# Optimization experiments

Measured on AMD Instinct MI355X. Metric: run time of the kernel, lower is better.

The kernel has to match this reference:

```python
import jax, jax.numpy as jnp
import numpy as np

DIM = 576
HEADS = 8
AGENT = 49
GRID_SIZE = 5
ORDER = 3
BN_EPS = 1e-5


def _kan_grid():
    h = 2.0 / GRID_SIZE  # grid_range [-1, 1]
    return jnp.arange(-ORDER, GRID_SIZE + ORDER + 1, dtype=jnp.float32) * h - 1.0


def _bsplines(x, grid):
    # x: (M, in) -> (M, in, GRID_SIZE + ORDER) Cox-de Boor B-spline bases (efficient-kan)
    xe = x[..., None]
    b = ((xe >= grid[:-1]) & (xe < grid[1:])).astype(x.dtype)
    for k in range(1, ORDER + 1):
        b = ((xe - grid[:-(k + 1)]) / (grid[k:-1] - grid[:-(k + 1)]) * b[..., :-1]
             + (grid[k + 1:] - xe) / (grid[k + 1:] - grid[1:-k]) * b[..., 1:])
    return b


def setup_inputs() -> dict:
    key = jax.random.key(0)
    ks = jax.random.split(key, 16)
    b, H, W = 32, 28, 28
    n, c = H * W, DIM
    nrm = lambda k, shape, std=0.02: jax.random.normal(k, shape, jnp.float32) * std
    return {
        "x": jax.random.normal(ks[0], (b, n, c), jnp.float32),
        "H": H,
        "W": W,
        "Wq": nrm(ks[1], (c, c)),
        "Wkv": nrm(ks[2], (2 * c, c)),
        "an_bias": nrm(ks[3], (HEADS, AGENT, 7, 7)),
        "na_bias": nrm(ks[4], (HEADS, AGENT, 7, 7)),
        "ah_bias": nrm(ks[5], (1, HEADS, AGENT, H, 1)),
        "aw_bias": nrm(ks[6], (1, HEADS, AGENT, 1, W)),
        "ha_bias": nrm(ks[7], (1, HEADS, H, 1, AGENT)),
        "wa_bias": nrm(ks[8], (1, HEADS, 1, W, AGENT)),
        "dwc_w": nrm(ks[9], (c, 1, 3, 3), 0.1),
        "dwc_b": jnp.zeros((c,), jnp.float32),
        "bn_gamma": jnp.ones((c,), jnp.float32),
        "bn_beta": jnp.zeros((c,), jnp.float32),
        "bn_mean": jnp.zeros((c,), jnp.float32),
        "bn_var": jnp.ones((c,), jnp.float32),
        "base_weight": nrm(ks[10], (c, c)),
        "spline_weight": nrm(ks[11], (c, c, GRID_SIZE + ORDER)),
        "spline_scaler": jnp.ones((c, c), jnp.float32),
    }


def reference(x, H, W, Wq, Wkv, an_bias, na_bias, ah_bias, aw_bias, ha_bias, wa_bias,
              dwc_w, dwc_b, bn_gamma, bn_beta, bn_mean, bn_var,
              base_weight, spline_weight, spline_scaler):
    b, n, c = x.shape
    h, hd = HEADS, c // HEADS
    scale = hd ** -0.5
    q = x @ Wq.T                       # (b,n,c)
    kv = x @ Wkv.T                     # (b,n,2c)  (sr_ratio == 1)
    k, v = kv[..., :c], kv[..., c:]
    # agent tokens: AdaptiveAvgPool2d(28x28 -> 7x7) == exact 4x4 mean pooling
    p = int(AGENT ** 0.5)
    agent = q.reshape(b, p, H // p, p, W // p, c).mean(axis=(2, 4)).reshape(b, AGENT, c)
    qh = q.reshape(b, n, h, hd).transpose(0, 2, 1, 3)       # (b,h,n,hd)
    kh = k.reshape(b, n, h, hd).transpose(0, 2, 1, 3)
    vh = v.reshape(b, n, h, hd).transpose(0, 2, 1, 3)
    ah = agent.reshape(b, AGENT, h, hd).transpose(0, 2, 1, 3)  # (b,h,A,hd)
    # stage 1: agent tokens attend to k/v (bilinear-upsampled 7x7 bias + separable bias)
    pb1 = jax.image.resize(an_bias, (h, AGENT, H, W), "bilinear").reshape(1, h, AGENT, n)
    pb2 = (ah_bias + aw_bias).reshape(1, h, AGENT, n)
    agent_attn = jax.nn.softmax(jnp.einsum("bhad,bhnd->bhan", ah * scale, kh) + pb1 + pb2, axis=-1)
    agent_v = jnp.einsum("bhan,bhnd->bhad", agent_attn, vh)    # (b,h,A,hd)
    # stage 2: queries attend to agent tokens
    ab1 = jax.image.resize(na_bias, (h, AGENT, H, W), "bilinear").reshape(1, h, AGENT, n).transpose(0, 1, 3, 2)
    ab2 = (ha_bias + wa_bias).reshape(1, h, n, AGENT)
    q_attn = jax.nn.softmax(jnp.einsum("bhnd,bhad->bhna", qh * scale, ah) + ab1 + ab2, axis=-1)
    out = jnp.einsum("bhna,bhad->bhnd", q_attn, agent_v).transpose(0, 2, 1, 3).reshape(b, n, c)
    # depthwise-conv + BN(eval) + ReLU residual on v
    vimg = v.transpose(0, 2, 1).reshape(b, c, H, W)
    y = jax.lax.conv_general_dilated(vimg, dwc_w, (1, 1), "SAME",
                                     feature_group_count=c,
                                     dimension_numbers=("NCHW", "OIHW", "NCHW"))
    y = y + dwc_b[None, :, None, None]
    scale_bn = (bn_gamma / jnp.sqrt(bn_var + BN_EPS))[None, :, None, None]
    y = (y - bn_mean[None, :, None, None]) * scale_bn + bn_beta[None, :, None, None]
    y = jax.nn.relu(y).reshape(b, c, n).transpose(0, 2, 1)
    out = out + y
    # KANLinear projection: silu base branch + B-spline branch
    xf = out.reshape(b * n, c)
    bases = _bsplines(xf, _kan_grid())                           # (M, in, 8)
    scaled = spline_weight * spline_scaler[..., None]            # (out, in, 8)
    proj = jax.nn.silu(xf) @ base_weight.T + jnp.einsum("mik,oik->mo", bases, scaled)
    return proj.reshape(b, n, c)
```

## Files before the change

kernel.cpp:

```cpp
#include <hip/hip_runtime.h>
#include <hip/hip_bf16.h>
#include <math.h>

#define B_ 32
#define N_ 784
#define C_ 576
#define H_ 28
#define W_ 28
#define HEADS_ 8
#define HD_ 72
#define AGENT_ 49
#define M_ (B_ * N_)
#define KTOT_ 5184
#define QKVW_ 1728
#define SCALE_ 0.11785113019775793f
#define LDA_ 40

typedef unsigned short ushort_t;
typedef __attribute__((ext_vector_type(8))) unsigned short u16x8;
typedef __attribute__((ext_vector_type(8))) __bf16 bf16x8;
typedef __attribute__((ext_vector_type(4))) float f32x4;
typedef __attribute__((ext_vector_type(4))) unsigned u32x4;

__device__ __forceinline__ ushort_t f2bf(float f) {
  union { float f; unsigned u; } v; v.f = f;
  unsigned r = v.u + 0x7fffu + ((v.u >> 16) & 1u);
  return (ushort_t)(r >> 16);
}
__device__ __forceinline__ float bf2f(ushort_t u) {
  union { unsigned u; float f; } v; v.u = ((unsigned)u) << 16;
  return v.f;
}
__device__ __forceinline__ unsigned pack2(float lo, float hi) {
  __bf16 a = (__bf16)lo, b = (__bf16)hi;
  unsigned short ua = __builtin_bit_cast(unsigned short, a);
  unsigned short ub = __builtin_bit_cast(unsigned short, b);
  return (unsigned)ua | ((unsigned)ub << 16);
}

__global__ __launch_bounds__(256) void convert_x_kernel(
    const float* __restrict__ x, ushort_t* __restrict__ xbf) {
  const int total8 = M_ * C_ / 8;
  for (int i = blockIdx.x * 256 + threadIdx.x; i < total8; i += gridDim.x * 256) {
    f32x4 a = *(const f32x4*)(x + i * 8);
    f32x4 b = *(const f32x4*)(x + i * 8 + 4);
    u16x8 o;
    o[0]=f2bf(a[0]); o[1]=f2bf(a[1]); o[2]=f2bf(a[2]); o[3]=f2bf(a[3]);
    o[4]=f2bf(b[0]); o[5]=f2bf(b[1]); o[6]=f2bf(b[2]); o[7]=f2bf(b[3]);
    *(u16x8*)(xbf + i * 8) = o;
  }
}

__global__ __launch_bounds__(256) void pack_w_kernel(
    const float* __restrict__ Wq, const float* __restrict__ Wkv,
    ushort_t* __restrict__ wbf) {
  int total = QKVW_ * C_;
  for (int i = blockIdx.x * 256 + threadIdx.x; i < total; i += gridDim.x * 256) {
    int j = i / C_, k = i % C_;
    float v = (j < C_) ? Wq[(size_t)j * C_ + k] : Wkv[(size_t)(j - C_) * C_ + k];
    wbf[i] = f2bf(v);
  }
}

__global__ __launch_bounds__(256) void pack_b_kernel(
    const float* __restrict__ base_w, const float* __restrict__ spline_w,
    const float* __restrict__ spline_s, ushort_t* __restrict__ bpackb) {
  int o = blockIdx.x;
  for (int j = threadIdx.x; j < KTOT_; j += 256) {
    float v;
    if (j < C_) {
      v = base_w[(size_t)o * C_ + j];
    } else {
      int jj = j - C_;
      int i = jj >> 3, kk = jj & 7;
      v = spline_w[((size_t)o * C_ + i) * 8 + kk] * spline_s[(size_t)o * C_ + i];
    }
    bpackb[(size_t)o * KTOT_ + j] = f2bf(v);
  }
}

__device__ __forceinline__ float bilerp7(const float* __restrict__ Bsrc, int y, int x) {
  float sy = y * 0.25f - 0.375f;
  float sx = x * 0.25f - 0.375f;
  float fy0 = floorf(sy), fx0 = floorf(sx);
  int y0 = (int)fy0, x0 = (int)fx0;
  float fy = sy - fy0, fx = sx - fx0;
  int y0c = min(6, max(0, y0)), y1c = min(6, max(0, y0 + 1));
  int x0c = min(6, max(0, x0)), x1c = min(6, max(0, x0 + 1));
  float v00 = Bsrc[y0c * 7 + x0c], v01 = Bsrc[y0c * 7 + x1c];
  float v10 = Bsrc[y1c * 7 + x0c], v11 = Bsrc[y1c * 7 + x1c];
  return (1.f - fy) * ((1.f - fx) * v00 + fx * v01)
       + fy * ((1.f - fx) * v10 + fx * v11);
}

__global__ __launch_bounds__(256) void bias_kernel(
    const float* __restrict__ an_bias, const float* __restrict__ na_bias,
    const float* __restrict__ ah_bias, const float* __restrict__ aw_bias,
    const float* __restrict__ ha_bias, const float* __restrict__ wa_bias,
    float* __restrict__ abias, float* __restrict__ qbias) {
  int idx = blockIdx.x * 256 + threadIdx.x;
  if (idx >= HEADS_ * AGENT_ * N_) return;
  int n = idx % N_;
  int ha = idx / N_;
  int h = ha / AGENT_, a = ha % AGENT_;
  int y = n / W_, x = n % W_;
  float pb1 = bilerp7(an_bias + (size_t)ha * 49, y, x);
  float pb2 = ah_bias[ha * H_ + y] + aw_bias[ha * W_ + x];
  abias[(size_t)ha * N_ + n] = pb1 + pb2;
  float ab1 = bilerp7(na_bias + (size_t)ha * 49, y, x);
  float ab2 = ha_bias[(h * H_ + y) * AGENT_ + a] + wa_bias[(h * W_ + x) * AGENT_ + a];
  qbias[((size_t)h * N_ + n) * AGENT_ + a] = ab1 + ab2;
}

__global__ __launch_bounds__(512, 4) void mfma_qkv_kernel(
    const ushort_t* __restrict__ A, const ushort_t* __restrict__ Bt,
    ushort_t* __restrict__ out) {
  __shared__ ushort_t Asl[2][128 * LDA_];
  __shared__ ushort_t Bsl[2][192 * LDA_];
  const int tid = threadIdx.x;
  const int lane = tid & 63, wid = tid >> 6;
  const int wm = wid >> 2, wn = wid & 3;
  const int l16 = lane & 15, lq = lane >> 4;

  int lin = blockIdx.x;
  const int q = 220, r = 4;
  int xcd = lin & 7;
  int wg = (xcd < r ? xcd * (q + 1) : r * (q + 1) + (xcd - r) * q) + (lin >> 3);
  const int m0 = (wg / 9) * 128, n0 = (wg % 9) * 192;

  const int rA = tid >> 2, hA = tid & 3;
  const int rB0 = tid >> 2, cB0 = tid & 3;
  const int rB1 = 128 + (tid >> 2), cB1 = tid & 3;
  const bool hasB1 = tid < 256;

  const ushort_t* arow = A + (size_t)(m0 + rA) * C_ + hA * 8;
  const ushort_t* brow0 = Bt + (size_t)(n0 + rB0) * C_ + cB0 * 8;
  const ushort_t* brow1 = Bt + (size_t)(n0 + rB1) * C_ + cB1 * 8;

  f32x4 acc[4][3] = {};
  u16x8 ar, br0, br1;

  ar = *(const u16x8*)(arow);
  br0 = *(const u16x8*)(brow0);
  if (hasB1) br1 = *(const u16x8*)(brow1);
  *(u16x8*)&Asl[0][rA * LDA_ + hA * 8] = ar;
  *(u16x8*)&Bsl[0][rB0 * LDA_ + cB0 * 8] = br0;
  if (hasB1) *(u16x8*)&Bsl[0][rB1 * LDA_ + cB1 * 8] = br1;
  ar = *(const u16x8*)(arow + 32);
  br0 = *(const u16x8*)(brow0 + 32);
  if (hasB1) br1 = *(const u16x8*)(brow1 + 32);
  __syncthreads();

  const int NSTEP = C_ / 32;
  for (int s = 0; s < NSTEP; ++s) {
    const int cur = s & 1;
    bf16x8 af[4], bfr[3];
    #pragma unroll
    for (int fm = 0; fm < 4; ++fm)
      af[fm] = *(const bf16x8*)&Asl[cur][(wm * 64 + fm * 16 + l16) * LDA_ + lq * 8];
    #pragma unroll
    for (int fn = 0; fn < 3; ++fn)
      bfr[fn] = *(const bf16x8*)&Bsl[cur][(wn * 48 + fn * 16 + l16) * LDA_ + lq * 8];
    #pragma unroll
    for (int fm = 0; fm < 4; ++fm)
      #pragma unroll
      for (int fn = 0; fn < 3; ++fn)
        acc[fm][fn] = __builtin_amdgcn_mfma_f32_16x16x32_bf16(
            af[fm], bfr[fn], acc[fm][fn], 0, 0, 0);
    if (s + 1 < NSTEP) {
      const int nxt = cur ^ 1;
      *(u16x8*)&Asl[nxt][rA * LDA_ + hA * 8] = ar;
      *(u16x8*)&Bsl[nxt][rB0 * LDA_ + cB0 * 8] = br0;
      if (hasB1) *(u16x8*)&Bsl[nxt][rB1 * LDA_ + cB1 * 8] = br1;
      if (s + 2 < NSTEP) {
        const int kl = (s + 2) * 32;
        ar = *(const u16x8*)(arow + kl);
        br0 = *(const u16x8*)(brow0 + kl);
        if (hasB1) br1 = *(const u16x8*)(brow1 + kl);
      }
    }
    __syncthreads();
  }
  #pragma unroll
  for (int fm = 0; fm < 4; ++fm) {
    #pragma unroll
    for (int fn = 0; fn < 3; ++fn) {
      int col = n0 + wn * 48 + fn * 16 + l16;
      #pragma unroll
      for (int r2 = 0; r2 < 4; ++r2) {
        int row = m0 + wm * 64 + fm * 16 + lq * 4 + r2;
        out[(size_t)row * QKVW_ + col] = f2bf(acc[fm][fn][r2]);
      }
    }
  }
}

__device__ __forceinline__ u32x4 basesPack(float xv) {
  float s = __fmaf_rn(xv, 2.5f, 5.5f);
  float tf = floorf(s);
  int t = (int)tf;
  float u = s - tf;
  float u2 = u * u, u3 = u2 * u, um = 1.f - u;
  float p0 = u3 * (1.f / 6.f);
  float p1 = (-3.f * u3 + 3.f * u2 + 3.f * u + 1.f) * (1.f / 6.f);
  float p2 = (3.f * u3 - 6.f * u2 + 4.f) * (1.f / 6.f);
  float p3 = um * um * um * (1.f / 6.f);
  unsigned lo = pack2(p3, p2);
  unsigned hi = pack2(p1, p0);
  unsigned cm1 = lo << 16;
  unsigned c1  = (lo >> 16) | (hi << 16);
  unsigned c3  = hi >> 16;
  bool inr = (t >= 0) && (t <= 10);
  u32x4 o;
  #pragma unroll
  for (int j = 0; j < 4; ++j) {
    int d = 3 - t + 2 * j;
    unsigned rr = 0u;
    rr = (d == -1) ? cm1 : rr;
    rr = (d == 0)  ? lo  : rr;
    rr = (d == 1)  ? c1  : rr;
    rr = (d == 2)  ? hi  : rr;
    rr = (d == 3)  ? c3  : rr;
    o[j] = inr ? rr : 0u;
  }
  return o;
}

__device__ __forceinline__ u32x4 siluPack(const float* xv) {
  u32x4 o;
  #pragma unroll
  for (int e = 0; e < 4; ++e) {
    float v0 = xv[2 * e], v1 = xv[2 * e + 1];
    float s0 = v0 / (1.f + __expf(-v0));
    float s1 = v1 / (1.f + __expf(-v1));
    o[e] = pack2(s0, s1);
  }
  return o;
}

__global__ __launch_bounds__(512, 4) void kan_mfma_kernel(
    const float* __restrict__ xf, const ushort_t* __restrict__ Bt,
    float* __restrict__ out) {
  __shared__ ushort_t Asl[2][128 * LDA_];
  __shared__ ushort_t Bsl[2][192 * LDA_];
  const int tid = threadIdx.x;
  const int lane = tid & 63, wid = tid >> 6;
  const int wm = wid >> 2, wn = wid & 3;
  const int l16 = lane & 15, lq = lane >> 4;

  int lin = blockIdx.x;
  const int q = 73, r = 4;
  int xcd = lin & 7;
  int wg = (xcd < r ? xcd * (q + 1) : r * (q + 1) + (xcd - r) * q) + (lin >> 3);
  const int m0 = (wg / 3) * 128, n0 = (wg % 3) * 192;

  const int rA = tid >> 2, hA = tid & 3;
  const int rB0 = tid >> 2, cB0 = tid & 3;
  const int rB1 = 128 + (tid >> 2), cB1 = tid & 3;
  const bool hasB1 = tid < 256;

  const float* xfr = xf + (size_t)(m0 + rA) * C_;
  const ushort_t* brow0 = Bt + (size_t)(n0 + rB0) * KTOT_ + cB0 * 8;
  const ushort_t* brow1 = Bt + (size_t)(n0 + rB1) * KTOT_ + cB1 * 8;

  f32x4 acc[4][3] = {};
  float xv[8];
  u16x8 br0, br1;

  {
    f32x4 a = *(const f32x4*)(xfr + hA * 8);
    f32x4 b = *(const f32x4*)(xfr + hA * 8 + 4);
    xv[0]=a[0]; xv[1]=a[1]; xv[2]=a[2]; xv[3]=a[3];
    xv[4]=b[0]; xv[5]=b[1]; xv[6]=b[2]; xv[7]=b[3];
  }
  br0 = *(const u16x8*)(brow0);
  if (hasB1) br1 = *(const u16x8*)(brow1);
  *(u32x4*)&Asl[0][rA * LDA_ + hA * 8] = siluPack(xv);
  *(u16x8*)&Bsl[0][rB0 * LDA_ + cB0 * 8] = br0;
  if (hasB1) *(u16x8*)&Bsl[0][rB1 * LDA_ + cB1 * 8] = br1;
  {
    f32x4 a = *(const f32x4*)(xfr + 32 + hA * 8);
    f32x4 b = *(const f32x4*)(xfr + 32 + hA * 8 + 4);
    xv[0]=a[0]; xv[1]=a[1]; xv[2]=a[2]; xv[3]=a[3];
    xv[4]=b[0]; xv[5]=b[1]; xv[6]=b[2]; xv[7]=b[3];
  }
  br0 = *(const u16x8*)(brow0 + 32);
  if (hasB1) br1 = *(const u16x8*)(brow1 + 32);
  __syncthreads();

  const int NSTEP = KTOT_ / 32;
  for (int s = 0; s < NSTEP; ++s) {
    const int cur = s & 1;
    bf16x8 af[4], bfr[3];
    #pragma unroll
    for (int fm = 0; fm < 4; ++fm)
      af[fm] = *(const bf16x8*)&Asl[cur][(wm * 64 + fm * 16 + l16) * LDA_ + lq * 8];
    #pragma unroll
    for (int fn = 0; fn < 3; ++fn)
      bfr[fn] = *(const bf16x8*)&Bsl[cur][(wn * 48 + fn * 16 + l16) * LDA_ + lq * 8];
    #pragma unroll
    for (int fm = 0; fm < 4; ++fm)
      #pragma unroll
      for (int fn = 0; fn < 3; ++fn)
        acc[fm][fn] = __builtin_amdgcn_mfma_f32_16x16x32_bf16(
            af[fm], bfr[fn], acc[fm][fn], 0, 0, 0);
    if (s + 1 < NSTEP) {
      const int nxt = cur ^ 1;
      const int kg = (s + 1) * 32;
      u32x4 a0 = (kg < C_) ? siluPack(xv) : basesPack(xv[0]);
      *(u32x4*)&Asl[nxt][rA * LDA_ + hA * 8] = a0;
      *(u16x8*)&Bsl[nxt][rB0 * LDA_ + cB0 * 8] = br0;
      if (hasB1) *(u16x8*)&Bsl[nxt][rB1 * LDA_ + cB1 * 8] = br1;
      if (s + 2 < NSTEP) {
        const int kl = (s + 2) * 32;
        if (kl < C_) {
          f32x4 a = *(const f32x4*)(xfr + kl + hA * 8);
          f32x4 b = *(const f32x4*)(xfr + kl + hA * 8 + 4);
          xv[0]=a[0]; xv[1]=a[1]; xv[2]=a[2]; xv[3]=a[3];
          xv[4]=b[0]; xv[5]=b[1]; xv[6]=b[2]; xv[7]=b[3];
        } else {
          xv[0] = xfr[((kl - C_) >> 3) + hA];
        }
        br0 = *(const u16x8*)(brow0 + kl);
        if (hasB1) br1 = *(const u16x8*)(brow1 + kl);
      }
    }
    __syncthreads();
  }
  #pragma unroll
  for (int fm = 0; fm < 4; ++fm) {
    #pragma unroll
    for (int fn = 0; fn < 3; ++fn) {
      int col = n0 + wn * 48 + fn * 16 + l16;
      #pragma unroll
      for (int r2 = 0; r2 < 4; ++r2) {
        int row = m0 + wm * 64 + fm * 16 + lq * 4 + r2;
        out[(size_t)row * C_ + col] = acc[fm][fn][r2];
      }
    }
  }
}

__global__ __launch_bounds__(576) void agent_pool_kernel(
    const ushort_t* __restrict__ qkvb, float* __restrict__ agent) {
  int ba = blockIdx.x;
  int b = ba / AGENT_, a = ba % AGENT_;
  int ay = a / 7, ax = a % 7;
  int ch = threadIdx.x;
  float s = 0.f;
  #pragma unroll
  for (int i2 = 0; i2 < 4; ++i2)
    #pragma unroll
    for (int i4 = 0; i4 < 4; ++i4)
      s += bf2f(qkvb[((size_t)b * N_ + (ay * 4 + i2) * W_ + (ax * 4 + i4)) * QKVW_ + ch]);
  agent[(size_t)ba * C_ + ch] = s * 0.0625f;
}

#define AKS_ 104
#define VTS_ 136
__global__ __launch_bounds__(256) void agent_attn_mfma_kernel(
    const float* __restrict__ agent, const ushort_t* __restrict__ qkvb,
    const float* __restrict__ abias, float* __restrict__ agent_v) {
  __shared__ ushort_t A_lds[64 * AKS_];
  __shared__ ushort_t K_lds[112 * AKS_];
  __shared__ ushort_t Vt_lds[80 * VTS_];
  __shared__ ushort_t P_lds[4][16 * VTS_];
  const int tid = threadIdx.x;
  const int lane = tid & 63, wid = tid >> 6;
  const int l16 = lane & 15, lq = lane >> 4;
  const int b = blockIdx.x >> 3, h = blockIdx.x & 7;

  for (int i = tid; i < 64 * AKS_; i += 256) A_lds[i] = 0;
  for (int i = tid; i < 112 * 32; i += 256) {
    int r = i >> 5, cc = 72 + (i & 31);
    K_lds[r * AKS_ + cc] = 0;
  }
  for (int i = tid; i < 80 * VTS_; i += 256) Vt_lds[i] = 0;
  for (int i = tid; i < 4 * 16 * 24; i += 256) {
    int w = i / (16 * 24), rest = i % (16 * 24);
    int r = rest / 24, cc = 112 + rest % 24;
    P_lds[w][r * VTS_ + cc] = 0;
  }
  for (int i = tid; i < AGENT_ * HD_; i += 256) {
    int a = i / HD_, d = i % HD_;
    A_lds[a * AKS_ + d] = f2bf(agent[((size_t)b * AGENT_ + a) * C_ + h * HD_ + d]);
  }

  int srow[4], scol[4]; bool sval[4];
  #pragma unroll
  for (int i = 0; i < 4; ++i) {
    int idx = tid + i * 256;
    srow[i] = idx / 9; scol[i] = idx % 9;
    sval[i] = idx < 1008;
  }
  const ushort_t* kbase = qkvb + (size_t)b * N_ * QKVW_ + C_ + h * HD_;
  const ushort_t* vbase = qkvb + (size_t)b * N_ * QKVW_ + 2 * C_ + h * HD_;

  u16x8 kreg[4], vreg[4];
  #pragma unroll
  for (int i = 0; i < 4; ++i) {
    if (sval[i]) {
      kreg[i] = *(const u16x8*)(kbase + (size_t)srow[i] * QKVW_ + scol[i] * 8);
      vreg[i] = *(const u16x8*)(vbase + (size_t)srow[i] * QKVW_ + scol[i] * 8);
    }
  }
  #pragma unroll
  for (int i = 0; i < 4; ++i) {
    if (sval[i]) {
      *(u16x8*)&K_lds[srow[i] * AKS_ + scol[i] * 8] = kreg[i];
      #pragma unroll
      for (int e = 0; e < 8; ++e)
        Vt_lds[(scol[i] * 8 + e) * VTS_ + srow[i]] = vreg[i][e];
    }
  }
  __syncthreads();

  float m_r[4] = {-1e30f, -1e30f, -1e30f, -1e30f};
  float l_r[4] = {};
  f32x4 O[5] = {};
  const float* bias_base[4];
  #pragma unroll
  for (int r = 0; r < 4; ++r) {
    int a = wid * 16 + lq * 4 + r;
    a = min(a, AGENT_ - 1);
    bias_base[r] = abias + ((size_t)h * AGENT_ + a) * N_;
  }

  for (int c = 0; c < 7; ++c) {
    if (c < 6) {
      const size_t off = (size_t)(c + 1) * 112 * QKVW_;
      #pragma unroll
      for (int i = 0; i < 4; ++i) {
        if (sval[i]) {
          kreg[i] = *(const u16x8*)(kbase + off + (size_t)srow[i] * QKVW_ + scol[i] * 8);
          vreg[i] = *(const u16x8*)(vbase + off + (size_t)srow[i] * QKVW_ + scol[i] * 8);
        }
      }
    }
    f32x4 sacc[7] = {};
    #pragma unroll
    for (int ks = 0; ks < 3; ++ks) {
      bf16x8 af = *(const bf16x8*)&A_lds[(wid * 16 + l16) * AKS_ + ks * 32 + lq * 8];
      #pragma unroll
      for (int nt = 0; nt < 7; ++nt) {
        bf16x8 bf = *(const bf16x8*)&K_lds[(nt * 16 + l16) * AKS_ + ks * 32 + lq * 8];
        sacc[nt] = __builtin_amdgcn_mfma_f32_16x16x32_bf16(af, bf, sacc[nt], 0, 0, 0);
      }
    }
    float cmax[4] = {-1e30f, -1e30f, -1e30f, -1e30f};
    const int nb = c * 112 + l16;
    #pragma unroll
    for (int nt = 0; nt < 7; ++nt)
      #pragma unroll
      for (int r = 0; r < 4; ++r) {
        float lg = sacc[nt][r] * SCALE_ + bias_base[r][nb + nt * 16];
        sacc[nt][r] = lg;
        cmax[r] = fmaxf(cmax[r], lg);
      }
    #pragma unroll
    for (int off = 1; off < 16; off <<= 1)
      #pragma unroll
      for (int r = 0; r < 4; ++r)
        cmax[r] = fmaxf(cmax[r], __shfl_xor(cmax[r], off));
    float scl[4], rs[4];
    #pragma unroll
    for (int r = 0; r < 4; ++r) {
      float nm = fmaxf(m_r[r], cmax[r]);
      scl[r] = __expf(m_r[r] - nm);
      m_r[r] = nm;
      rs[r] = 0.f;
    }
    #pragma unroll
    for (int nt = 0; nt < 7; ++nt)
      #pragma unroll
      for (int r = 0; r < 4; ++r) {
        float p = __expf(sacc[nt][r] - m_r[r]);
        rs[r] += p;
        P_lds[wid][(lq * 4 + r) * VTS_ + nt * 16 + l16] = f2bf(p);
      }
    #pragma unroll
    for (int off = 1; off < 16; off <<= 1)
      #pragma unroll
      for (int r = 0; r < 4; ++r)
        rs[r] += __shfl_xor(rs[r], off);
    #pragma unroll
    for (int r = 0; r < 4; ++r) l_r[r] = l_r[r] * scl[r] + rs[r];
    #pragma unroll
    for (int nt = 0; nt < 5; ++nt)
      #pragma unroll
      for (int r = 0; r < 4; ++r) O[nt][r] *= scl[r];
    #pragma unroll
    for (int ks = 0; ks < 4; ++ks) {
      bf16x8 pf = *(const bf16x8*)&P_lds[wid][l16 * VTS_ + ks * 32 + lq * 8];
      #pragma unroll
      for (int nt = 0; nt < 5; ++nt) {
        bf16x8 vf = *(const bf16x8*)&Vt_lds[(nt * 16 + l16) * VTS_ + ks * 32 + lq * 8];
        O[nt] = __builtin_amdgcn_mfma_f32_16x16x32_bf16(pf, vf, O[nt], 0, 0, 0);
      }
    }
    __syncthreads();
    if (c < 6) {
      #pragma unroll
      for (int i = 0; i < 4; ++i) {
        if (sval[i]) {
          *(u16x8*)&K_lds[srow[i] * AKS_ + scol[i] * 8] = kreg[i];
          #pragma unroll
          for (int e = 0; e < 8; ++e)
            Vt_lds[(scol[i] * 8 + e) * VTS_ + srow[i]] = vreg[i][e];
        }
      }
      __syncthreads();
    }
  }
  float inv[4];
  #pragma unroll
  for (int r = 0; r < 4; ++r) inv[r] = 1.f / l_r[r];
  #pragma unroll
  for (int nt = 0; nt < 5; ++nt) {
    int d = nt * 16 + l16;
    if (d >= HD_) continue;
    #pragma unroll
    for (int r = 0; r < 4; ++r) {
      int a = wid * 16 + lq * 4 + r;
      if (a < AGENT_)
        agent_v[(((size_t)b * HEADS_ + h) * AGENT_ + a) * HD_ + d] = O[nt][r] * inv[r];
    }
  }
}

__global__ __launch_bounds__(256) void q_attn_kernel(
    const ushort_t* __restrict__ qkvb, const float* __restrict__ agent,
    const float* __restrict__ agent_v, const float* __restrict__ qbias,
    float* __restrict__ xf) {
  __shared__ float ag_t[HD_ * 52];
  __shared__ float av_t[HD_ * 52];
  const int tid = threadIdx.x;
  const int h = blockIdx.y, b = blockIdx.z;
  for (int t = tid; t < AGENT_ * HD_; t += 256) {
    int a = t / HD_, d = t % HD_;
    ag_t[d * 52 + a] = agent[((size_t)b * AGENT_ + a) * C_ + h * HD_ + d];
    av_t[d * 52 + a] = agent_v[(((size_t)b * HEADS_ + h) * AGENT_ + a) * HD_ + d];
  }
  __syncthreads();
  const int n = blockIdx.x * 256 + tid;
  if (n >= N_) return;
  const ushort_t* qp = qkvb + ((size_t)b * N_ + n) * QKVW_ + h * HD_;
  const float* qb = qbias + ((size_t)h * N_ + n) * AGENT_;
  float lg[AGENT_];
  #pragma unroll
  for (int a = 0; a < AGENT_; ++a) lg[a] = qb[a];
  for (int d = 0; d < HD_; ++d) {
    float qd = bf2f(qp[d]) * SCALE_;
    #pragma unroll
    for (int a = 0; a < AGENT_; ++a) lg[a] += qd * ag_t[d * 52 + a];
  }
  float mx = -1e30f;
  #pragma unroll
  for (int a = 0; a < AGENT_; ++a) mx = fmaxf(mx, lg[a]);
  float s = 0.f;
  #pragma unroll
  for (int a = 0; a < AGENT_; ++a) { lg[a] = __expf(lg[a] - mx); s += lg[a]; }
  float inv = 1.f / s;
  #pragma unroll
  for (int a = 0; a < AGENT_; ++a) lg[a] *= inv;
  float* op = xf + ((size_t)b * N_ + n) * C_ + h * HD_;
  for (int d = 0; d < HD_; ++d) {
    float acc = 0.f;
    #pragma unroll
    for (int a = 0; a < AGENT_; ++a) acc += lg[a] * av_t[d * 52 + a];
    op[d] = acc;
  }
}

__global__ __launch_bounds__(288) void dwc_kernel(
    const ushort_t* __restrict__ qkvb, const float* __restrict__ w,
    const float* __restrict__ bias, const float* __restrict__ gamma,
    const float* __restrict__ beta, const float* __restrict__ mean,
    const float* __restrict__ var, float* __restrict__ xf) {
  const int bn = blockIdx.x;
  const int b = bn / N_, n = bn % N_;
  const int y = n / W_, x = n % W_;
  const int c0 = threadIdx.x * 2;
  float a0 = 0.f, a1 = 0.f;
  #pragma unroll
  for (int ky = 0; ky < 3; ++ky) {
    int yy = y + ky - 1;
    if (yy < 0 || yy >= H_) continue;
    #pragma unroll
    for (int kx = 0; kx < 3; ++kx) {
      int xx = x + kx - 1;
      if (xx < 0 || xx >= W_) continue;
      unsigned v = *(const unsigned*)(qkvb + ((size_t)b * N_ + yy * W_ + xx) * QKVW_ + 2 * C_ + c0);
      a0 += w[c0 * 9 + ky * 3 + kx] * bf2f((ushort_t)(v & 0xffffu));
      a1 += w[(c0 + 1) * 9 + ky * 3 + kx] * bf2f((ushort_t)(v >> 16));
    }
  }
  float s0 = gamma[c0] * rsqrtf(var[c0] + 1e-5f);
  float s1 = gamma[c0 + 1] * rsqrtf(var[c0 + 1] + 1e-5f);
  float r0 = fmaxf((a0 + bias[c0] - mean[c0]) * s0 + beta[c0], 0.f);
  float r1 = fmaxf((a1 + bias[c0 + 1] - mean[c0 + 1]) * s1 + beta[c0 + 1], 0.f);
  float2* xp = (float2*)&xf[(size_t)bn * C_ + c0];
  float2 old = *xp;
  old.x += r0; old.y += r1;
  *xp = old;
}

extern "C" void kernel_launch(void* const* d_in, const int* in_sizes, int n_in,
                              void* d_out, int out_size, void* d_ws, size_t ws_size,
                              hipStream_t stream) {
  const float* x        = (const float*)d_in[0];
  const float* Wq       = (const float*)d_in[3];
  const float* Wkv      = (const float*)d_in[4];
  const float* an_bias  = (const float*)d_in[5];
  const float* na_bias  = (const float*)d_in[6];
  const float* ah_bias  = (const float*)d_in[7];
  const float* aw_bias  = (const float*)d_in[8];
  const float* ha_bias  = (const float*)d_in[9];
  const float* wa_bias  = (const float*)d_in[10];
  const float* dwc_w    = (const float*)d_in[11];
  const float* dwc_b    = (const float*)d_in[12];
  const float* bn_gamma = (const float*)d_in[13];
  const float* bn_beta  = (const float*)d_in[14];
  const float* bn_mean  = (const float*)d_in[15];
  const float* bn_var   = (const float*)d_in[16];
  const float* base_w   = (const float*)d_in[17];
  const float* spline_w = (const float*)d_in[18];
  const float* spline_s = (const float*)d_in[19];

  char* ws = (char*)d_ws;
  ushort_t* qkvb   = (ushort_t*)(ws + 0);
  ushort_t* xbf    = (ushort_t*)(ws + 86704128);
  ushort_t* wbf    = (ushort_t*)(ws + 115605504);
  ushort_t* bpackb = (ushort_t*)(ws + 117596160);
  float* agent     = (float*)(ws + 123568128);
  float* agent_v   = (float*)(ws + 127180800);
  float* abias     = (float*)(ws + 130793472);
  float* qbias     = (float*)(ws + 132022784);
  float* xf        = (float*)(ws + 133252096);
  float* out       = (float*)d_out;

  convert_x_kernel<<<dim3(2048), dim3(256), 0, stream>>>(x, xbf);
  pack_w_kernel<<<dim3(1024), dim3(256), 0, stream>>>(Wq, Wkv, wbf);
  pack_b_kernel<<<dim3(C_), dim3(256), 0, stream>>>(base_w, spline_w, spline_s, bpackb);
  bias_kernel<<<dim3((HEADS_ * AGENT_ * N_ + 255) / 256), dim3(256), 0, stream>>>(
      an_bias, na_bias, ah_bias, aw_bias, ha_bias, wa_bias, abias, qbias);
  mfma_qkv_kernel<<<dim3(1764), dim3(512), 0, stream>>>(xbf, wbf, qkvb);
  agent_pool_kernel<<<dim3(B_ * AGENT_), dim3(C_), 0, stream>>>(qkvb, agent);
  agent_attn_mfma_kernel<<<dim3(B_ * HEADS_), dim3(256), 0, stream>>>(
      agent, qkvb, abias, agent_v);
  q_attn_kernel<<<dim3(4, HEADS_, B_), dim3(256), 0, stream>>>(
      qkvb, agent, agent_v, qbias, xf);
  dwc_kernel<<<dim3(M_), dim3(288), 0, stream>>>(
      qkvb, dwc_w, dwc_b, bn_gamma, bn_beta, bn_mean, bn_var, xf);
  kan_mfma_kernel<<<dim3(588), dim3(512), 0, stream>>>(xf, bpackb, out);
}
```

Before: 672.0 us.

## Swizzle LDS tiles instead of padding, raise occupancy bound, simplify spline packing

Replaces the padded LDS row stride (40) with a dense 32-element stride and an XOR swizzle, so bank conflicts stay low while shared memory per block shrinks. The smaller footprint allows launch_bounds to go from 4 to 6 blocks per CU for both GEMM kernels. The B-spline basis packing drops its per-lane select chain in favour of 64-bit shifts and FMA-form polynomials. Risks are register pressure from the tighter launch bound and subtle errors in the shift logic.

```diff
diff --git a/kernel.cpp b/kernel.cpp
--- a/kernel.cpp
+++ b/kernel.cpp
@@ -14,7 +14,8 @@
 #define KTOT_ 5184
 #define QKVW_ 1728
 #define SCALE_ 0.11785113019775793f
-#define LDA_ 40
+
+#define SWZ(row, chunk) (((row) << 5) + ((((chunk) ^ (((row) >> 1) & 3))) << 3))
 
 typedef unsigned short ushort_t;
 typedef __attribute__((ext_vector_type(8))) unsigned short u16x8;
@@ -112,11 +113,11 @@
   qbias[((size_t)h * N_ + n) * AGENT_ + a] = ab1 + ab2;
 }
 
-__global__ __launch_bounds__(512, 4) void mfma_qkv_kernel(
+__global__ __launch_bounds__(512, 6) void mfma_qkv_kernel(
     const ushort_t* __restrict__ A, const ushort_t* __restrict__ Bt,
     ushort_t* __restrict__ out) {
-  __shared__ ushort_t Asl[2][128 * LDA_];
-  __shared__ ushort_t Bsl[2][192 * LDA_];
+  __shared__ ushort_t Asl[2][128 * 32];
+  __shared__ ushort_t Bsl[2][192 * 32];
   const int tid = threadIdx.x;
   const int lane = tid & 63, wid = tid >> 6;
   const int wm = wid >> 2, wn = wid & 3;
@@ -137,15 +138,19 @@
   const ushort_t* brow0 = Bt + (size_t)(n0 + rB0) * C_ + cB0 * 8;
   const ushort_t* brow1 = Bt + (size_t)(n0 + rB1) * C_ + cB1 * 8;
 
+  const int aWo = SWZ(rA, hA);
+  const int b0Wo = SWZ(rB0, cB0);
+  const int b1Wo = SWZ(rB1, cB1);
+
   f32x4 acc[4][3] = {};
   u16x8 ar, br0, br1;
 
   ar = *(const u16x8*)(arow);
   br0 = *(const u16x8*)(brow0);
   if (hasB1) br1 = *(const u16x8*)(brow1);
-  *(u16x8*)&Asl[0][rA * LDA_ + hA * 8] = ar;
-  *(u16x8*)&Bsl[0][rB0 * LDA_ + cB0 * 8] = br0;
-  if (hasB1) *(u16x8*)&Bsl[0][rB1 * LDA_ + cB1 * 8] = br1;
+  *(u16x8*)&Asl[0][aWo] = ar;
+  *(u16x8*)&Bsl[0][b0Wo] = br0;
+  if (hasB1) *(u16x8*)&Bsl[0][b1Wo] = br1;
   ar = *(const u16x8*)(arow + 32);
   br0 = *(const u16x8*)(brow0 + 32);
   if (hasB1) br1 = *(const u16x8*)(brow1 + 32);
@@ -157,10 +162,10 @@
     bf16x8 af[4], bfr[3];
     #pragma unroll
     for (int fm = 0; fm < 4; ++fm)
-      af[fm] = *(const bf16x8*)&Asl[cur][(wm * 64 + fm * 16 + l16) * LDA_ + lq * 8];
+      af[fm] = *(const bf16x8*)&Asl[cur][SWZ(wm * 64 + fm * 16 + l16, lq)];
     #pragma unroll
     for (int fn = 0; fn < 3; ++fn)
-      bfr[fn] = *(const bf16x8*)&Bsl[cur][(wn * 48 + fn * 16 + l16) * LDA_ + lq * 8];
+      bfr[fn] = *(const bf16x8*)&Bsl[cur][SWZ(wn * 48 + fn * 16 + l16, lq)];
     #pragma unroll
     for (int fm = 0; fm < 4; ++fm)
       #pragma unroll
@@ -169,9 +174,9 @@
             af[fm], bfr[fn], acc[fm][fn], 0, 0, 0);
     if (s + 1 < NSTEP) {
       const int nxt = cur ^ 1;
-      *(u16x8*)&Asl[nxt][rA * LDA_ + hA * 8] = ar;
-      *(u16x8*)&Bsl[nxt][rB0 * LDA_ + cB0 * 8] = br0;
-      if (hasB1) *(u16x8*)&Bsl[nxt][rB1 * LDA_ + cB1 * 8] = br1;
+      *(u16x8*)&Asl[nxt][aWo] = ar;
+      *(u16x8*)&Bsl[nxt][b0Wo] = br0;
+      if (hasB1) *(u16x8*)&Bsl[nxt][b1Wo] = br1;
       if (s + 2 < NSTEP) {
         const int kl = (s + 2) * 32;
         ar = *(const u16x8*)(arow + kl);
@@ -202,27 +207,24 @@
   float u = s - tf;
   float u2 = u * u, u3 = u2 * u, um = 1.f - u;
   float p0 = u3 * (1.f / 6.f);
-  float p1 = (-3.f * u3 + 3.f * u2 + 3.f * u + 1.f) * (1.f / 6.f);
-  float p2 = (3.f * u3 - 6.f * u2 + 4.f) * (1.f / 6.f);
+  float p1 = __fmaf_rn(u3, -0.5f, __fmaf_rn(u2, 0.5f, __fmaf_rn(u, 0.5f, 1.f / 6.f)));
+  float p2 = __fmaf_rn(u3, 0.5f, __fmaf_rn(u2, -1.f, 2.f / 3.f));
   float p3 = um * um * um * (1.f / 6.f);
   unsigned lo = pack2(p3, p2);
   unsigned hi = pack2(p1, p0);
-  unsigned cm1 = lo << 16;
-  unsigned c1  = (lo >> 16) | (hi << 16);
-  unsigned c3  = hi >> 16;
-  bool inr = (t >= 0) && (t <= 10);
+  unsigned long long packed = ((unsigned long long)hi << 32) | (unsigned long long)lo;
+  int sh = t - 3;
+  int ba = sh << 4;
+  unsigned long long shl_lo = packed << (ba & 63);
+  unsigned long long shr_sp = packed >> ((64 - ba) & 63);
+  unsigned long long shl_hi = packed << ((ba - 64) & 63);
+  unsigned long long shr_ng = packed >> ((-ba) & 63);
+  unsigned long long Olo = (sh < 0) ? shr_ng : ((sh < 4) ? shl_lo : 0ull);
+  unsigned long long Ohi = (sh <= 0) ? 0ull : ((sh < 4) ? shr_sp : shl_hi);
+  if (t < 0 || t > 10) { Olo = 0ull; Ohi = 0ull; }
   u32x4 o;
-  #pragma unroll
-  for (int j = 0; j < 4; ++j) {
-    int d = 3 - t + 2 * j;
-    unsigned rr = 0u;
-    rr = (d == -1) ? cm1 : rr;
-    rr = (d == 0)  ? lo  : rr;
-    rr = (d == 1)  ? c1  : rr;
-    rr = (d == 2)  ? hi  : rr;
-    rr = (d == 3)  ? c3  : rr;
-    o[j] = inr ? rr : 0u;
-  }
+  o[0] = (unsigned)Olo; o[1] = (unsigned)(Olo >> 32);
+  o[2] = (unsigned)Ohi; o[3] = (unsigned)(Ohi >> 32);
   return o;
 }
 
@@ -238,11 +240,11 @@
   return o;
 }
 
-__global__ __launch_bounds__(512, 4) void kan_mfma_kernel(
+__global__ __launch_bounds__(512, 6) void kan_mfma_kernel(
     const float* __restrict__ xf, const ushort_t* __restrict__ Bt,
     float* __restrict__ out) {
-  __shared__ ushort_t Asl[2][128 * LDA_];
-  __shared__ ushort_t Bsl[2][192 * LDA_];
+  __shared__ ushort_t Asl[2][128 * 32];
+  __shared__ ushort_t Bsl[2][192 * 32];
   const int tid = threadIdx.x;
   const int lane = tid & 63, wid = tid >> 6;
   const int wm = wid >> 2, wn = wid & 3;
@@ -263,6 +265,10 @@
   const ushort_t* brow0 = Bt + (size_t)(n0 + rB0) * KTOT_ + cB0 * 8;
   const ushort_t* brow1 = Bt + (size_t)(n0 + rB1) * KTOT_ + cB1 * 8;
 
+  const int aWo = SWZ(rA, hA);
+  const int b0Wo = SWZ(rB0, cB0);
+  const int b1Wo = SWZ(rB1, cB1);
+
   f32x4 acc[4][3] = {};
   float xv[8];
   u16x8 br0, br1;
@@ -275,9 +281,9 @@
   }
   br0 = *(const u16x8*)(brow0);
   if (hasB1) br1 = *(const u16x8*)(brow1);
-  *(u32x4*)&Asl[0][rA * LDA_ + hA * 8] = siluPack(xv);
-  *(u16x8*)&Bsl[0][rB0 * LDA_ + cB0 * 8] = br0;
-  if (hasB1) *(u16x8*)&Bsl[0][rB1 * LDA_ + cB1 * 8] = br1;
+  *(u32x4*)&Asl[0][aWo] = siluPack(xv);
+  *(u16x8*)&Bsl[0][b0Wo] = br0;
+  if (hasB1) *(u16x8*)&Bsl[0][b1Wo] = br1;
   {
     f32x4 a = *(const f32x4*)(xfr + 32 + hA * 8);
     f32x4 b = *(const f32x4*)(xfr + 32 + hA * 8 + 4);
@@ -294,10 +300,10 @@
     bf16x8 af[4], bfr[3];
     #pragma unroll
     for (int fm = 0; fm < 4; ++fm)
-      af[fm] = *(const bf16x8*)&Asl[cur][(wm * 64 + fm * 16 + l16) * LDA_ + lq * 8];
+      af[fm] = *(const bf16x8*)&Asl[cur][SWZ(wm * 64 + fm * 16 + l16, lq)];
     #pragma unroll
     for (int fn = 0; fn < 3; ++fn)
-      bfr[fn] = *(const bf16x8*)&Bsl[cur][(wn * 48 + fn * 16 + l16) * LDA_ + lq * 8];
+      bfr[fn] = *(const bf16x8*)&Bsl[cur][SWZ(wn * 48 + fn * 16 + l16, lq)];
     #pragma unroll
     for (int fm = 0; fm < 4; ++fm)
       #pragma unroll
@@ -308,9 +314,9 @@
       const int nxt = cur ^ 1;
       const int kg = (s + 1) * 32;
       u32x4 a0 = (kg < C_) ? siluPack(xv) : basesPack(xv[0]);
-      *(u32x4*)&Asl[nxt][rA * LDA_ + hA * 8] = a0;
-      *(u16x8*)&Bsl[nxt][rB0 * LDA_ + cB0 * 8] = br0;
-      if (hasB1) *(u16x8*)&Bsl[nxt][rB1 * LDA_ + cB1 * 8] = br1;
+      *(u32x4*)&Asl[nxt][aWo] = a0;
+      *(u16x8*)&Bsl[nxt][b0Wo] = br0;
+      if (hasB1) *(u16x8*)&Bsl[nxt][b1Wo] = br1;
       if (s + 2 < NSTEP) {
         const int kl = (s + 2) * 32;
         if (kl < C_) {
```

Measured after the change: 1.308 ms. 1.95x slower.
